# Kernel tuning notes

Hardware: AMD Instinct MI355X
Metric: run time of the kernel (lower is better)

Reference implementation:

```python
import jax, jax.numpy as jnp
import numpy as np

HIDDEN = 64

def setup_inputs() -> dict:
    key = jax.random.key(0)
    ks = jax.random.split(key, 10)
    B, E = 8, 200000
    h = jax.random.normal(ks[0], (B, E, HIDDEN), dtype=jnp.float32)
    J = jax.random.normal(ks[1], (B, E, 1), dtype=jnp.float32)
    b_in = jax.random.normal(ks[2], (B, E, 1), dtype=jnp.float32)
    b_out = jax.random.normal(ks[3], (B, E, 1), dtype=jnp.float32)
    d_in = HIDDEN + 4
    # PyTorch Linear default init: U(-1/sqrt(fan_in), 1/sqrt(fan_in))
    def lin(kw, kb, fan_in, fan_out):
        bound = 1.0 / np.sqrt(fan_in)
        W = jax.random.uniform(kw, (fan_in, fan_out), minval=-bound, maxval=bound, dtype=jnp.float32)
        b = jax.random.uniform(kb, (fan_out,), minval=-bound, maxval=bound, dtype=jnp.float32)
        return W, b
    W1, b1 = lin(ks[4], ks[5], d_in, 64)
    W2, b2 = lin(ks[6], ks[7], 64, 64)
    W3, b3 = lin(ks[8], ks[9], 64, 5)
    return {"h": h, "J": J, "b_in": b_in, "b_out": b_out,
            "W1": W1, "b1": b1, "W2": W2, "b2": b2, "W3": W3, "b3": b3}

def reference(h, J, b_in, b_out, W1, b1, W2, b2, W3, b3):
    # concat order matches torch.cat((h, b_in, b_out, J, -J), 2)
    x = jnp.concatenate((h, b_in, b_out, J, -J), axis=2)  # [B,E,hidden+4]
    x = jax.nn.relu(jnp.einsum('bei,io->beo', x, W1) + b1)
    x = jax.nn.relu(jnp.einsum('bei,io->beo', x, W2) + b2)
    message = jnp.einsum('bei,io->beo', x, W3) + b3  # [B,E,5]
    return message
```

## Files before the change

### kernel.cpp

```cpp
#include <hip/hip_runtime.h>

typedef __bf16 bf16x8 __attribute__((ext_vector_type(8)));
typedef float  f32x4  __attribute__((ext_vector_type(4)));

#define MFMA(A, B, C) __builtin_amdgcn_mfma_f32_16x16x32_bf16((A), (B), (C), 0, 0, 0)

__global__ __launch_bounds__(256, 4)
void msg_mlp(const float* __restrict__ hbuf, const float* __restrict__ Jbuf,
             const float* __restrict__ binb, const float* __restrict__ boutb,
             const float* __restrict__ W1, const float* __restrict__ b1,
             const float* __restrict__ W2, const float* __restrict__ b2,
             const float* __restrict__ W3, const float* __restrict__ b3,
             float* __restrict__ out, int n_rows, int n_tiles)
{
    __shared__ __align__(16) char wlds[27 * 1024];
    const int lane = threadIdx.x & 63;
    const int e = lane & 15;
    const int q = lane >> 4;
    const int wv = (int)(threadIdx.x >> 6);
    const int wid = blockIdx.x * 4 + wv;
    const int nw  = gridDim.x * 4;
    char* slot = wlds + lane * 16;

    if (wv == 0) {
#pragma unroll
      for (int mt = 0; mt < 4; ++mt)
#pragma unroll
        for (int kk = 0; kk < 2; ++kk) {
          bf16x8 v;
#pragma unroll
          for (int i = 0; i < 8; ++i)
            v[i] = (__bf16)W1[(16*q + 8*kk + i)*64 + 16*mt + e];
          *(bf16x8*)(slot + (mt*2 + kk) * 1024) = v;
        }
#pragma unroll
      for (int mt = 0; mt < 4; ++mt) {
        const int o = 16*mt + e;
        float w0;
        if      (q == 0) w0 =  W1[64*64 + o];
        else if (q == 1) w0 =  W1[65*64 + o];
        else if (q == 2) w0 =  W1[66*64 + o];
        else             w0 = -W1[67*64 + o];
        bf16x8 v;
        v[0] = (__bf16)w0;
        v[1] = (q == 0) ? (__bf16)b1[o] : (__bf16)0.0f;
#pragma unroll
        for (int i = 2; i < 8; ++i) v[i] = (__bf16)0.0f;
        *(bf16x8*)(slot + (8 + mt) * 1024) = v;
      }
    } else if (wv == 1) {
#pragma unroll
      for (int mt = 0; mt < 4; ++mt)
#pragma unroll
        for (int kk = 0; kk < 2; ++kk) {
          bf16x8 v;
#pragma unroll
          for (int i = 0; i < 8; ++i) {
            const int f = 16*(2*kk + (i>>2)) + 4*q + (i&3);
            v[i] = (__bf16)W2[f*64 + 16*mt + e];
          }
          *(bf16x8*)(slot + (12 + mt*2 + kk) * 1024) = v;
        }
    } else if (wv == 2) {
#pragma unroll
      for (int kk = 0; kk < 2; ++kk) {
        bf16x8 v;
#pragma unroll
        for (int i = 0; i < 8; ++i) {
          const int f = 16*(2*kk + (i>>2)) + 4*q + (i&3);
          v[i] = (e < 5) ? (__bf16)W3[f*5 + e] : (__bf16)0.0f;
        }
        *(bf16x8*)(slot + (20 + kk) * 1024) = v;
      }
      f32x4 v3;
#pragma unroll
      for (int r = 0; r < 4; ++r) v3[r] = (4*q + r < 5) ? b3[4*q + r] : 0.0f;
      *(f32x4*)(slot + 26 * 1024) = v3;
    } else {
#pragma unroll
      for (int mt = 0; mt < 4; ++mt) {
        f32x4 v;
#pragma unroll
        for (int r = 0; r < 4; ++r) v[r] = b2[16*mt + 4*q + r];
        *(f32x4*)(slot + (22 + mt) * 1024) = v;
      }
    }

    const float* sptr = (q == 0) ? binb : (q == 1) ? boutb : Jbuf;
    const __bf16 biasf = (q == 0) ? (__bf16)1.0f : (__bf16)0.0f;

    __syncthreads();

#pragma unroll 1
    for (int t = wid; t < n_tiles; t += nw) {
      int z0 = 0;
      asm volatile("" : "+s"(z0));
      const char* Wf = slot + z0;

      int re = t * 16 + e;
      if (re >= n_rows) re = n_rows - 1;
      const float* hr = hbuf + (size_t)re * 64 + q * 16;
      const f32x4 v0 = *(const f32x4*)(hr);
      const f32x4 v1 = *(const f32x4*)(hr + 4);
      const f32x4 v2 = *(const f32x4*)(hr + 8);
      const f32x4 v3 = *(const f32x4*)(hr + 12);
      const float s  = sptr[re];

      bf16x8 xb0, xb1, xb2;
#pragma unroll
      for (int i = 0; i < 4; ++i) {
        xb0[i]     = (__bf16)v0[i];
        xb0[i + 4] = (__bf16)v1[i];
        xb1[i]     = (__bf16)v2[i];
        xb1[i + 4] = (__bf16)v3[i];
      }
      xb2[0] = (__bf16)s; xb2[1] = biasf;
#pragma unroll
      for (int i = 2; i < 8; ++i) xb2[i] = (__bf16)0.0f;

      f32x4 acc1[4];
#pragma unroll
      for (int mt = 0; mt < 4; ++mt) {
        const bf16x8 wa = *(const bf16x8*)(Wf + (mt*2 + 0) * 1024);
        const bf16x8 wb = *(const bf16x8*)(Wf + (mt*2 + 1) * 1024);
        const bf16x8 wx = *(const bf16x8*)(Wf + (8 + mt)  * 1024);
        acc1[mt] = (f32x4){0.f, 0.f, 0.f, 0.f};
        acc1[mt] = MFMA(wa, xb0, acc1[mt]);
        acc1[mt] = MFMA(wb, xb1, acc1[mt]);
        acc1[mt] = MFMA(wx, xb2, acc1[mt]);
      }
      bf16x8 y[2];
#pragma unroll
      for (int kk = 0; kk < 2; ++kk)
#pragma unroll
        for (int i = 0; i < 8; ++i)
          y[kk][i] = (__bf16)fmaxf(acc1[2*kk + (i>>2)][i & 3], 0.0f);

      f32x4 acc2[4];
#pragma unroll
      for (int mt = 0; mt < 4; ++mt) {
        const bf16x8 wa = *(const bf16x8*)(Wf + (12 + mt*2 + 0) * 1024);
        const bf16x8 wb = *(const bf16x8*)(Wf + (12 + mt*2 + 1) * 1024);
        acc2[mt] = *(const f32x4*)(Wf + (22 + mt) * 1024);
        acc2[mt] = MFMA(wa, y[0], acc2[mt]);
        acc2[mt] = MFMA(wb, y[1], acc2[mt]);
      }
      bf16x8 z[2];
#pragma unroll
      for (int kk = 0; kk < 2; ++kk)
#pragma unroll
        for (int i = 0; i < 8; ++i)
          z[kk][i] = (__bf16)fmaxf(acc2[2*kk + (i>>2)][i & 3], 0.0f);

      f32x4 acc3 = *(const f32x4*)(Wf + 26 * 1024);
      acc3 = MFMA(*(const bf16x8*)(Wf + 20 * 1024), z[0], acc3);
      acc3 = MFMA(*(const bf16x8*)(Wf + 21 * 1024), z[1], acc3);

      const int rowi = t * 16 + e;
      if (rowi < n_rows) {
        float* orow = out + (size_t)rowi * 5;
        if (q == 0) {
          orow[0] = acc3[0]; orow[1] = acc3[1];
          orow[2] = acc3[2]; orow[3] = acc3[3];
        } else if (q == 1) {
          orow[4] = acc3[0];
        }
      }
    }
}

extern "C" void kernel_launch(void* const* d_in, const int* in_sizes, int n_in,
                              void* d_out, int out_size, void* d_ws, size_t ws_size,
                              hipStream_t stream) {
    const float* h     = (const float*)d_in[0];
    const float* J     = (const float*)d_in[1];
    const float* b_in  = (const float*)d_in[2];
    const float* b_out = (const float*)d_in[3];
    const float* W1    = (const float*)d_in[4];
    const float* b1    = (const float*)d_in[5];
    const float* W2    = (const float*)d_in[6];
    const float* b2    = (const float*)d_in[7];
    const float* W3    = (const float*)d_in[8];
    const float* b3    = (const float*)d_in[9];
    float* out = (float*)d_out;

    const int n_rows  = in_sizes[1];
    const int n_tiles = (n_rows + 15) / 16;

    dim3 grid(1024), block(256);
    hipLaunchKernelGGL(msg_mlp, grid, block, 0, stream,
                       h, J, b_in, b_out, W1, b1, W2, b2, W3, b3,
                       out, n_rows, n_tiles);
}
```

Baseline: 92.55 us.

## Compact LDS bias layout and use 512-thread blocks with balanced grid

```diff
diff --git a/kernel.cpp b/kernel.cpp
--- a/kernel.cpp
+++ b/kernel.cpp
@@ -5,7 +5,9 @@
 
 #define MFMA(A, B, C) __builtin_amdgcn_mfma_f32_16x16x32_bf16((A), (B), (C), 0, 0, 0)
 
-__global__ __launch_bounds__(256, 4)
+#define B2_OFF 22528
+#define B3_OFF 22784
+__global__ __launch_bounds__(512, 8)
 void msg_mlp(const float* __restrict__ hbuf, const float* __restrict__ Jbuf,
              const float* __restrict__ binb, const float* __restrict__ boutb,
              const float* __restrict__ W1, const float* __restrict__ b1,
@@ -13,13 +15,13 @@
              const float* __restrict__ W3, const float* __restrict__ b3,
              float* __restrict__ out, int n_rows, int n_tiles)
 {
-    __shared__ __align__(16) char wlds[27 * 1024];
+    __shared__ __align__(16) char wlds[22848];
     const int lane = threadIdx.x & 63;
     const int e = lane & 15;
     const int q = lane >> 4;
     const int wv = (int)(threadIdx.x >> 6);
-    const int wid = blockIdx.x * 4 + wv;
-    const int nw  = gridDim.x * 4;
+    const int wid = blockIdx.x * 8 + wv;
+    const int nw  = gridDim.x * 8;
     char* slot = wlds + lane * 16;
 
     if (wv == 0) {
@@ -72,18 +74,11 @@
         }
         *(bf16x8*)(slot + (20 + kk) * 1024) = v;
       }
-      f32x4 v3;
-#pragma unroll
-      for (int r = 0; r < 4; ++r) v3[r] = (4*q + r < 5) ? b3[4*q + r] : 0.0f;
-      *(f32x4*)(slot + 26 * 1024) = v3;
-    } else {
-#pragma unroll
-      for (int mt = 0; mt < 4; ++mt) {
-        f32x4 v;
-#pragma unroll
-        for (int r = 0; r < 4; ++r) v[r] = b2[16*mt + 4*q + r];
-        *(f32x4*)(slot + (22 + mt) * 1024) = v;
-      }
+    } else if (wv == 3) {
+      ((float*)(wlds + B2_OFF))[lane] = b2[lane];
+    } else if (wv == 4) {
+      if (lane < 16)
+        ((float*)(wlds + B3_OFF))[lane] = (lane < 5) ? b3[lane] : 0.0f;
     }
 
     const float* sptr = (q == 0) ? binb : (q == 1) ? boutb : Jbuf;
@@ -96,6 +91,7 @@
       int z0 = 0;
       asm volatile("" : "+s"(z0));
       const char* Wf = slot + z0;
+      const char* Wb = wlds + 16*q + z0;
 
       int re = t * 16 + e;
       if (re >= n_rows) re = n_rows - 1;
@@ -141,7 +137,7 @@
       for (int mt = 0; mt < 4; ++mt) {
         const bf16x8 wa = *(const bf16x8*)(Wf + (12 + mt*2 + 0) * 1024);
         const bf16x8 wb = *(const bf16x8*)(Wf + (12 + mt*2 + 1) * 1024);
-        acc2[mt] = *(const f32x4*)(Wf + (22 + mt) * 1024);
+        acc2[mt] = *(const f32x4*)(Wb + B2_OFF + 64*mt);
         acc2[mt] = MFMA(wa, y[0], acc2[mt]);
         acc2[mt] = MFMA(wb, y[1], acc2[mt]);
       }
@@ -152,7 +148,7 @@
         for (int i = 0; i < 8; ++i)
           z[kk][i] = (__bf16)fmaxf(acc2[2*kk + (i>>2)][i & 3], 0.0f);
 
-      f32x4 acc3 = *(const f32x4*)(Wf + 26 * 1024);
+      f32x4 acc3 = *(const f32x4*)(Wb + B3_OFF);
       acc3 = MFMA(*(const bf16x8*)(Wf + 20 * 1024), z[0], acc3);
       acc3 = MFMA(*(const bf16x8*)(Wf + 21 * 1024), z[1], acc3);
 
@@ -187,7 +183,12 @@
     const int n_rows  = in_sizes[1];
     const int n_tiles = (n_rows + 15) / 16;
 
-    dim3 grid(1024), block(256);
+    const int MAXW   = 8192;
+    const int iters  = (n_tiles + MAXW - 1) / MAXW;
+    const int waves  = (n_tiles + iters - 1) / iters;
+    const int blocks = (waves + 7) / 8;
+
+    dim3 grid(blocks), block(512);
     hipLaunchKernelGGL(msg_mlp, grid, block, 0, stream,
                        h, J, b_in, b_out, W1, b1, W2, b2, W3, b3,
                        out, n_rows, n_tiles);
```

Result: slower. 102.4 us (+10.7%).
